# Performance work log

Hardware: AMD Instinct MI355X
Metric: run time of the kernel (lower is better)

## Reference

```python
import jax, jax.numpy as jnp
import numpy as np

EPS = 1e-5

def group_points(feat, idx):
    # feat: [B, C, N1], idx: [B, N2, K] -> [B, C, N2, K]
    return jax.vmap(lambda f, i: f[:, i])(feat, idx)

def conv_bn_relu(x, W, gamma, beta):
    # 1x1 conv2d (no bias) + training-mode BatchNorm2d + ReLU
    y = jnp.einsum('oc,bcnk->bonk', W, x)
    mean = y.mean(axis=(0, 2, 3), keepdims=True)
    var = y.var(axis=(0, 2, 3), keepdims=True)  # biased, as BN uses for normalization
    y = (y - mean) * jax.lax.rsqrt(var + EPS)
    y = y * gamma[None, :, None, None] + beta[None, :, None, None]
    return jax.nn.relu(y)

def setup_inputs() -> dict:
    key = jax.random.key(0)
    ks = jax.random.split(key, 12)
    B, N1, N2, K, C1 = 16, 4096, 1024, 32, 64
    mlp = [C1 + 3, 64, 64, 128]  # use_xyz adds 3 channels
    inp = {
        'in_xyz': jax.random.normal(ks[0], (B, 3, N1), jnp.float32),
        'out_xyz': jax.random.normal(ks[1], (B, 3, N2), jnp.float32),
        'in_feature': jax.random.normal(ks[2], (B, C1, N1), jnp.float32),
        'nbr_index': jax.random.randint(ks[3], (B, N2, K), 0, N1, jnp.int32),
    }
    for li in range(3):
        cin, cout = mlp[li], mlp[li + 1]
        inp[f'W{li}'] = jax.random.normal(ks[4 + li], (cout, cin), jnp.float32) * (1.0 / np.sqrt(cin))
        inp[f'g{li}'] = jnp.ones((cout,), jnp.float32)
        inp[f'b{li}'] = jnp.zeros((cout,), jnp.float32)
    return inp

def reference(in_xyz, out_xyz, in_feature, nbr_index,
              W0, g0, b0, W1, g1, b1, W2, g2, b2):
    # gather neighbor features: [B, C1, N2, K]
    nbr_feature = group_points(in_feature, nbr_index)
    # gather neighbor xyz, recenter on query points: [B, 3, N2, K]
    nbr_xyz = group_points(in_xyz, nbr_index) - out_xyz[:, :, :, None]
    x = jnp.concatenate([nbr_feature, nbr_xyz], axis=1)  # [B, C1+3, N2, K]
    x = conv_bn_relu(x, W0, g0, b0)
    x = conv_bn_relu(x, W1, g1, b1)
    x = conv_bn_relu(x, W2, g2, b2)
    return jnp.max(x, axis=3)  # [B, C2, N2]
```

## Files before the change

### kernel.cpp

```cpp
#include <hip/hip_runtime.h>
#include <cstdint>

typedef unsigned short u16;
typedef unsigned int   u32;
typedef __attribute__((ext_vector_type(8))) short  short8;
typedef __attribute__((ext_vector_type(4))) float  floatx4;

#define NPTS 524288

__device__ __forceinline__ float b2f(u16 h) { return __uint_as_float(((u32)h) << 16); }
__device__ __forceinline__ u16 f2b(float f) {
  u32 u = __float_as_uint(f);
  return (u16)((u + 0x7FFFu + ((u >> 16) & 1u)) >> 16);
}
__device__ __forceinline__ u32 pk_bf16(float lo, float hi) {
  return (u32)f2b(lo) | ((u32)f2b(hi) << 16);
}
__device__ __forceinline__ short8 ld_frag8(const u16* p) {
  union { uint4 q; short8 s; } x;
  x.q = *(const uint4*)p;
  return x.s;
}
__device__ __forceinline__ void bar_lds() {
  asm volatile("s_waitcnt lgkmcnt(0)\n\ts_barrier" ::: "memory");
}

__global__ __launch_bounds__(256) void prep_all(const float* __restrict__ inf,
                                                const float* __restrict__ ixyz,
                                                const float* __restrict__ W0,
                                                const float* __restrict__ W1,
                                                const float* __restrict__ W2,
                                                u16* __restrict__ featT,
                                                float4* __restrict__ xyzT,
                                                u16* __restrict__ Wb) {
  __shared__ float tile[32 * 33];
  const int bk = blockIdx.x, t = threadIdx.x;
  if (bk < 4096) {
    int b = bk >> 8, rem = bk & 255, cc = rem >> 7, nc = rem & 127;
    #pragma unroll
    for (int i = 0; i < 4; ++i) {
      int flat = t + i * 256;
      int cl = flat >> 5, nl = flat & 31;
      tile[cl * 33 + nl] = inf[(size_t)((b * 64) + cc * 32 + cl) * 4096 + nc * 32 + nl];
    }
    __syncthreads();
    #pragma unroll
    for (int i = 0; i < 4; ++i) {
      int flat = t + i * 256;
      int nl = flat >> 5, cl = flat & 31;
      featT[(size_t)((b << 12) + nc * 32 + nl) * 64 + cc * 32 + cl] = f2b(tile[cl * 33 + nl]);
    }
  } else if (bk < 4352) {
    int g = (bk - 4096) * 256 + t;
    int b = g >> 12, n = g & 4095;
    const float* p = ixyz + (size_t)b * 12288;
    xyzT[g] = make_float4(p[n], p[4096 + n], p[8192 + n], 0.f);
  } else {
    int s = (bk - 4352) * 256 + t;
    u16 v = 0;
    if (s < 6656)       { int o = s / 104, c = s % 104; if (c < 67) v = f2b(W0[o * 67 + c]); }
    else if (s < 11264) { int q = s - 6656;  int o = q / 72, c = q % 72; if (c < 64) v = f2b(W1[o * 64 + c]); }
    else                { int q = s - 11264; int o = q / 72, c = q % 72; if (c < 64) v = f2b(W2[o * 64 + c]); }
    Wb[s] = v;
  }
}

template<int KSTEPS, int OCH, bool GATHER, bool MAXOUT>
__global__ __launch_bounds__(256, 4) void gemm_layer(
    const u16* __restrict__ xsrc, const float4* __restrict__ xyzT,
    const float* __restrict__ oxyz, const int* __restrict__ nbr,
    const u16* __restrict__ Wb, const float* __restrict__ ssin,
    u16* __restrict__ yout, u32* __restrict__ gm,
    float* __restrict__ partial) {
  constexpr int PITCH = KSTEPS * 32 + 8;
  __shared__ __align__(16) u16 xs[2][64 * PITCH];
  __shared__ float red[512];
  __shared__ float ss[GATHER ? 4 : 128];

  const int t = threadIdx.x, blk = blockIdx.x;
  const int lane = t & 63, wv = t >> 6, lr = lane & 15, quad = lane >> 4;
  const int m = t >> 2, s4 = t & 3;
  const int P0 = blk * 256;
  const int b = blk >> 7;
  const int rg = wv >> 1, cg = wv & 1;

  short8 wf[4][KSTEPS];
  #pragma unroll
  for (int nt = 0; nt < 4; ++nt) {
    const int orow = (MAXOUT ? cg * 64 : 0) + nt * 16 + lr;
    const u16* wr = Wb + orow * PITCH + quad * 8;
    #pragma unroll
    for (int ks = 0; ks < KSTEPS; ++ks)
      wf[nt][ks] = ld_frag8(wr + ks * 32);
  }

  if constexpr (!GATHER) {
    if (t < 128) ss[t] = ssin[t];
  }
  if constexpr (GATHER) {
    #pragma unroll
    for (int bu = 0; bu < 2; ++bu) {
      if (s4 == 1) {
        u16* xr = xs[bu] + m * PITCH;
        xr[67] = 0;
        #pragma unroll
        for (int j = 0; j < 9; ++j) *(uint2*)(xr + 68 + j * 4) = make_uint2(0u, 0u);
      }
    }
  }
  if constexpr (!GATHER) __syncthreads();

  int idx4[4];
  if constexpr (GATHER) {
    #pragma unroll
    for (int sub = 0; sub < 4; ++sub) idx4[sub] = nbr[P0 + sub * 64 + m];
  }

  uint4 f0, f1;
  float DX = 0.f, DY = 0.f, DZ = 0.f;

  auto issue = [&](int sub) {
    const int P = P0 + sub * 64 + m;
    if constexpr (GATHER) {
      const int id = idx4[sub];
      const u16* row = xsrc + ((size_t)((b << 12) + id)) * 64;
      f0 = *(const uint4*)(row + s4 * 16);
      f1 = *(const uint4*)(row + s4 * 16 + 8);
      if (s4 == 0) {
        const int n2 = (P & 32767) >> 5;
        float4 p = xyzT[(b << 12) + id];
        DX = p.x - oxyz[(b * 3 + 0) * 1024 + n2];
        DY = p.y - oxyz[(b * 3 + 1) * 1024 + n2];
        DZ = p.z - oxyz[(b * 3 + 2) * 1024 + n2];
      }
    } else {
      const u16* row = xsrc + ((size_t)P << 6);
      f0 = *(const uint4*)(row + s4 * 16);
      f1 = *(const uint4*)(row + s4 * 16 + 8);
    }
  };

  auto commit = [&](int bu) {
    u16* xrow = xs[bu] + m * PITCH + s4 * 16;
    if constexpr (GATHER) {
      *(uint4*)(xrow + 0) = f0;
      *(uint4*)(xrow + 8) = f1;
      if (s4 == 0) {
        u16* xr = xs[bu] + m * PITCH;
        xr[64] = f2b(DX); xr[65] = f2b(DY); xr[66] = f2b(DZ);
      }
    } else {
      u32 w[8] = { f0.x, f0.y, f0.z, f0.w, f1.x, f1.y, f1.z, f1.w };
      u32 o[8];
      #pragma unroll
      for (int i = 0; i < 8; ++i) {
        const int c = s4 * 16 + i * 2;
        float lo = fmaxf(b2f((u16)(w[i] & 0xffffu)) * ss[c]     + ss[64 + c],     0.f);
        float hi = fmaxf(b2f((u16)(w[i] >> 16))     * ss[c + 1] + ss[64 + c + 1], 0.f);
        o[i] = pk_bf16(lo, hi);
      }
      *(uint4*)(xrow + 0) = make_uint4(o[0], o[1], o[2], o[3]);
      *(uint4*)(xrow + 8) = make_uint4(o[4], o[5], o[6], o[7]);
    }
  };

  issue(0); commit(0);
  issue(1);
  __syncthreads();

  float s1[4] = {0.f, 0.f, 0.f, 0.f}, s2[4] = {0.f, 0.f, 0.f, 0.f};
  u32* yo = (u32*)yout;

  for (int sub = 0; sub < 4; ++sub) {
    const int cur = sub & 1;
    if (sub < 3) commit(cur ^ 1);
    if (sub < 2) issue(sub + 2);

    if constexpr (!MAXOUT) {
      const u16* ap = xs[cur] + (wv * 16 + lr) * PITCH + quad * 8;
      floatx4 acc[4];
      #pragma unroll
      for (int nt = 0; nt < 4; ++nt) acc[nt] = (floatx4){0.f, 0.f, 0.f, 0.f};
      #pragma unroll
      for (int ks = 0; ks < KSTEPS; ++ks) {
        short8 av = ld_frag8(ap + ks * 32);
        #pragma unroll
        for (int nt = 0; nt < 4; ++nt)
          acc[nt] = __builtin_amdgcn_mfma_f32_16x16x32_bf16(av, wf[nt][ks], acc[nt], 0, 0, 0);
      }
      const int R0 = P0 + sub * 64 + wv * 16 + quad * 4;
      #pragma unroll
      for (int nt = 0; nt < 4; ++nt) {
        #pragma unroll
        for (int r = 0; r < 4; ++r) {
          float v = acc[nt][r];
          s1[nt] += v; s2[nt] += v * v;
          float vo = __shfl_xor(v, 1);
          if ((lr & 1) == 0)
            yo[(size_t)(R0 + r) * 32 + nt * 8 + (lr >> 1)] = pk_bf16(v, vo);
        }
      }
    } else {
      short8 av[2][KSTEPS];
      #pragma unroll
      for (int h = 0; h < 2; ++h)
        #pragma unroll
        for (int ks = 0; ks < KSTEPS; ++ks)
          av[h][ks] = ld_frag8(xs[cur] + (rg * 32 + h * 16 + lr) * PITCH + quad * 8 + ks * 32);
      floatx4 acc[2][4];
      #pragma unroll
      for (int h = 0; h < 2; ++h)
        #pragma unroll
        for (int nt = 0; nt < 4; ++nt) acc[h][nt] = (floatx4){0.f, 0.f, 0.f, 0.f};
      #pragma unroll
      for (int ks = 0; ks < KSTEPS; ++ks)
        #pragma unroll
        for (int nt = 0; nt < 4; ++nt)
          #pragma unroll
          for (int h = 0; h < 2; ++h)
            acc[h][nt] = __builtin_amdgcn_mfma_f32_16x16x32_bf16(av[h][ks], wf[nt][ks], acc[h][nt], 0, 0, 0);
      float mx[4], mn[4];
      #pragma unroll
      for (int nt = 0; nt < 4; ++nt) {
        mx[nt] = -INFINITY; mn[nt] = INFINITY;
        #pragma unroll
        for (int h = 0; h < 2; ++h)
          #pragma unroll
          for (int r = 0; r < 4; ++r) {
            float v = acc[h][nt][r];
            s1[nt] += v; s2[nt] += v * v;
            mx[nt] = fmaxf(mx[nt], v); mn[nt] = fminf(mn[nt], v);
          }
        mx[nt] = fmaxf(mx[nt], __shfl_xor(mx[nt], 16));
        mx[nt] = fmaxf(mx[nt], __shfl_xor(mx[nt], 32));
        mn[nt] = fminf(mn[nt], __shfl_xor(mn[nt], 16));
        mn[nt] = fminf(mn[nt], __shfl_xor(mn[nt], 32));
      }
      if (lane < 16) {
        const int grp = blk * 8 + sub * 2 + rg;
        #pragma unroll
        for (int nt = 0; nt < 4; ++nt)
          gm[(size_t)grp * 128 + cg * 64 + nt * 16 + lr] = pk_bf16(mx[nt], mn[nt]);
      }
    }
    if (sub < 3) bar_lds();
  }

  #pragma unroll
  for (int nt = 0; nt < 4; ++nt) {
    s1[nt] += __shfl_xor(s1[nt], 16); s1[nt] += __shfl_xor(s1[nt], 32);
    s2[nt] += __shfl_xor(s2[nt], 16); s2[nt] += __shfl_xor(s2[nt], 32);
  }
  if (lane < 16) {
    #pragma unroll
    for (int nt = 0; nt < 4; ++nt) {
      red[wv * 64 + nt * 16 + lr] = s1[nt];
      red[256 + wv * 64 + nt * 16 + lr] = s2[nt];
    }
  }
  __syncthreads();
  if constexpr (!MAXOUT) {
    if (t < 64) {
      partial[(size_t)blk * 128 + t] = red[t] + red[64 + t] + red[128 + t] + red[192 + t];
    } else if (t < 128) {
      int c = t - 64;
      partial[(size_t)blk * 128 + t] = red[256 + c] + red[320 + c] + red[384 + c] + red[448 + c];
    }
  } else {
    if (t < 128) {
      int half = t >> 6, i = t & 63;
      partial[(size_t)blk * 256 + t] = red[half * 64 + i] + red[(half + 2) * 64 + i];
    } else {
      int c = t - 128, half = c >> 6, i = c & 63;
      partial[(size_t)blk * 256 + t] = red[256 + half * 64 + i] + red[256 + (half + 2) * 64 + i];
    }
  }
}

__global__ __launch_bounds__(256) void reduce1(const float* __restrict__ partial,
                                               float* __restrict__ tmp, int cols) {
  int c = threadIdx.x;
  if (c >= cols) return;
  int r0 = blockIdx.x * 32;
  float s = 0.f;
  for (int r = 0; r < 32; ++r) s += partial[(size_t)(r0 + r) * cols + c];
  tmp[blockIdx.x * cols + c] = s;
}

__global__ __launch_bounds__(256) void finalize2(const float* __restrict__ tmp,
                                                 const float* __restrict__ gam,
                                                 const float* __restrict__ bet,
                                                 float* __restrict__ ssout, int och) {
  __shared__ float l[256];
  int t = threadIdx.x, cols = 2 * och;
  if (t < cols) {
    float s = 0.f;
    for (int r = 0; r < 64; ++r) s += tmp[r * cols + t];
    l[t] = s;
  }
  __syncthreads();
  if (t < och) {
    const float invN = 1.f / (float)NPTS;
    float mean = l[t] * invN;
    float var  = fmaxf(l[och + t] * invN - mean * mean, 0.f);
    float scale = gam[t] * rsqrtf(var + 1e-5f);
    ssout[t] = scale;
    ssout[och + t] = bet[t] - mean * scale;
  }
}

__global__ __launch_bounds__(256) void final_out(const u32* __restrict__ gm,
                                                 const float* __restrict__ ss2,
                                                 float* __restrict__ out) {
  __shared__ float tile[64 * 33];
  int blk = blockIdx.x;
  int b = blk >> 6, rem = blk & 63, cc = rem >> 4, nn = rem & 15;
  int t = threadIdx.x;
  #pragma unroll
  for (int i = 0; i < 8; ++i) {
    int flat = t + i * 256;
    int n2l = flat >> 5, cl = flat & 31;
    int c = cc * 32 + cl;
    size_t idx = (size_t)((b << 10) + nn * 64 + n2l) * 128 + c;
    u32 p = gm[idx];
    float mx = b2f((u16)(p & 0xffffu)), mn = b2f((u16)(p >> 16));
    float scv = ss2[c], shv = ss2[128 + c];
    float v = (scv >= 0.f) ? mx : mn;
    tile[n2l * 33 + cl] = fmaxf(scv * v + shv, 0.f);
  }
  __syncthreads();
  #pragma unroll
  for (int i = 0; i < 8; ++i) {
    int flat = t + i * 256;
    int cl = flat >> 6, n2l = flat & 63;
    out[(size_t)((b * 128) + cc * 32 + cl) * 1024 + nn * 64 + n2l] = tile[n2l * 33 + cl];
  }
}

extern "C" void kernel_launch(void* const* d_in, const int* in_sizes, int n_in,
                              void* d_out, int out_size, void* d_ws, size_t ws_size,
                              hipStream_t stream) {
  const float* in_xyz  = (const float*)d_in[0];
  const float* out_xyz = (const float*)d_in[1];
  const float* in_feat = (const float*)d_in[2];
  const int*   nbr     = (const int*)d_in[3];
  const float* W0 = (const float*)d_in[4];
  const float* g0 = (const float*)d_in[5];
  const float* b0 = (const float*)d_in[6];
  const float* W1 = (const float*)d_in[7];
  const float* g1 = (const float*)d_in[8];
  const float* b1 = (const float*)d_in[9];
  const float* W2 = (const float*)d_in[10];
  const float* g2 = (const float*)d_in[11];
  const float* b2 = (const float*)d_in[12];
  float* out = (float*)d_out;

  char* ws = (char*)d_ws;
  float*  ssbuf = (float*)(ws + 0);
  u16*    Wb    = (u16*)(ws + 4096);
  float*  tmpA  = (float*)(ws + 65536);
  u16*    featT = (u16*)(ws + 262144);
  float4* xyzT  = (float4*)(ws + 8650752);
  u16*    y0    = (u16*)(ws + 9699328);
  u16*    y1    = (u16*)(ws + 76808192);
  float*  p0    = (float*)(ws + 76808192);
  float*  p1    = (float*)(ws + 262144);
  u32*    gm    = (u32*)(ws + 9699328);
  float*  p2    = (float*)(ws + 9699328 + 8388608);

  hipLaunchKernelGGL(prep_all, dim3(4432), dim3(256), 0, stream,
                     in_feat, in_xyz, W0, W1, W2, featT, xyzT, Wb);

  hipLaunchKernelGGL((gemm_layer<3, 64, true, false>), dim3(2048), dim3(256), 0, stream,
                     featT, xyzT, out_xyz, nbr, Wb, nullptr, y0, nullptr, p0);
  hipLaunchKernelGGL(reduce1, dim3(64), dim3(256), 0, stream, p0, tmpA, 128);
  hipLaunchKernelGGL(finalize2, dim3(1), dim3(256), 0, stream, tmpA, g0, b0, ssbuf, 64);

  hipLaunchKernelGGL((gemm_layer<2, 64, false, false>), dim3(2048), dim3(256), 0, stream,
                     y0, nullptr, nullptr, nullptr, Wb + 6656, ssbuf, y1, nullptr, p1);
  hipLaunchKernelGGL(reduce1, dim3(64), dim3(256), 0, stream, p1, tmpA, 128);
  hipLaunchKernelGGL(finalize2, dim3(1), dim3(256), 0, stream, tmpA, g1, b1, ssbuf + 256, 64);

  hipLaunchKernelGGL((gemm_layer<2, 128, false, true>), dim3(2048), dim3(256), 0, stream,
                     y1, nullptr, nullptr, nullptr, Wb + 11264, ssbuf + 256, nullptr, gm, p2);
  hipLaunchKernelGGL(reduce1, dim3(64), dim3(256), 0, stream, p2, tmpA, 256);
  hipLaunchKernelGGL(finalize2, dim3(1), dim3(256), 0, stream, tmpA, g2, b2, ssbuf + 512, 128);

  hipLaunchKernelGGL(final_out, dim3(1024), dim3(256), 0, stream, gm, ssbuf + 512, out);
}
```

Before: 207.1 us.

## Precompute recentered xyz, deepen gather prefetch, fuse BN reduce and finalize

prep_all now gathers neighbor xyz, subtracts the query point and stores packed bf16 dx/dy/dz per point. The first GEMM then loads one uint2 per row instead of doing a dependent xyzT gather plus three oxyz loads. The gemm loader issues three subtiles ahead through a three-slot register ring so more global loads are in flight. The reduce1 and finalize2 pair is merged into one bn_stats kernel that uses atomicAdd and a last-block counter, removing three launches. In exchange it uses more registers, adds a 4 MB intermediate, and the atomic accumulation order makes the float sums nondeterministic.

```diff
diff --git a/kernel.cpp b/kernel.cpp
--- a/kernel.cpp
+++ b/kernel.cpp
@@ -27,12 +27,16 @@
 
 __global__ __launch_bounds__(256) void prep_all(const float* __restrict__ inf,
                                                 const float* __restrict__ ixyz,
+                                                const float* __restrict__ oxyz,
+                                                const int* __restrict__ nbr,
                                                 const float* __restrict__ W0,
                                                 const float* __restrict__ W1,
                                                 const float* __restrict__ W2,
                                                 u16* __restrict__ featT,
-                                                float4* __restrict__ xyzT,
-                                                u16* __restrict__ Wb) {
+                                                uint2* __restrict__ dxyz,
+                                                u16* __restrict__ Wb,
+                                                u32* __restrict__ cnt,
+                                                float* __restrict__ accz) {
   __shared__ float tile[32 * 33];
   const int bk = blockIdx.x, t = threadIdx.x;
   if (bk < 4096) {
@@ -50,25 +54,35 @@
       int nl = flat >> 5, cl = flat & 31;
       featT[(size_t)((b << 12) + nc * 32 + nl) * 64 + cc * 32 + cl] = f2b(tile[cl * 33 + nl]);
     }
-  } else if (bk < 4352) {
+  } else if (bk < 6144) {
     int g = (bk - 4096) * 256 + t;
-    int b = g >> 12, n = g & 4095;
-    const float* p = ixyz + (size_t)b * 12288;
-    xyzT[g] = make_float4(p[n], p[4096 + n], p[8192 + n], 0.f);
+    int b = g >> 15, r = g & 32767, n2 = r >> 5;
+    int id = nbr[g];
+    const float* ix = ixyz + (size_t)b * 12288;
+    const float* ox = oxyz + (size_t)b * 3072;
+    float dx = ix[id]        - ox[n2];
+    float dy = ix[4096 + id] - ox[1024 + n2];
+    float dzv = ix[8192 + id] - ox[2048 + n2];
+    dxyz[g] = make_uint2(pk_bf16(dx, dy), pk_bf16(dzv, 0.f));
   } else {
-    int s = (bk - 4352) * 256 + t;
+    int s = (bk - 6144) * 256 + t;
     u16 v = 0;
     if (s < 6656)       { int o = s / 104, c = s % 104; if (c < 67) v = f2b(W0[o * 67 + c]); }
     else if (s < 11264) { int q = s - 6656;  int o = q / 72, c = q % 72; if (c < 64) v = f2b(W1[o * 64 + c]); }
     else                { int q = s - 11264; int o = q / 72, c = q % 72; if (c < 64) v = f2b(W2[o * 64 + c]); }
     Wb[s] = v;
+    if (bk == 6144) {
+      if (t < 4) cnt[t] = 0u;
+      accz[t] = 0.f;
+      accz[256 + t] = 0.f;
+    }
   }
 }
 
 template<int KSTEPS, int OCH, bool GATHER, bool MAXOUT>
 __global__ __launch_bounds__(256, 4) void gemm_layer(
-    const u16* __restrict__ xsrc, const float4* __restrict__ xyzT,
-    const float* __restrict__ oxyz, const int* __restrict__ nbr,
+    const u16* __restrict__ xsrc, const uint2* __restrict__ dxyz,
+    const int* __restrict__ nbr,
     const u16* __restrict__ Wb, const float* __restrict__ ssin,
     u16* __restrict__ yout, u32* __restrict__ gm,
     float* __restrict__ partial) {
@@ -102,7 +116,6 @@
     for (int bu = 0; bu < 2; ++bu) {
       if (s4 == 1) {
         u16* xr = xs[bu] + m * PITCH;
-        xr[67] = 0;
         #pragma unroll
         for (int j = 0; j < 9; ++j) *(uint2*)(xr + 68 + j * 4) = make_uint2(0u, 0u);
       }
@@ -116,41 +129,33 @@
     for (int sub = 0; sub < 4; ++sub) idx4[sub] = nbr[P0 + sub * 64 + m];
   }
 
-  uint4 f0, f1;
-  float DX = 0.f, DY = 0.f, DZ = 0.f;
-
-  auto issue = [&](int sub) {
+  uint4 f0[3], f1[3];
+  uint2 dz[3];
+
+  auto issue = [&](int sub, int st) {
     const int P = P0 + sub * 64 + m;
     if constexpr (GATHER) {
       const int id = idx4[sub];
       const u16* row = xsrc + ((size_t)((b << 12) + id)) * 64;
-      f0 = *(const uint4*)(row + s4 * 16);
-      f1 = *(const uint4*)(row + s4 * 16 + 8);
-      if (s4 == 0) {
-        const int n2 = (P & 32767) >> 5;
-        float4 p = xyzT[(b << 12) + id];
-        DX = p.x - oxyz[(b * 3 + 0) * 1024 + n2];
-        DY = p.y - oxyz[(b * 3 + 1) * 1024 + n2];
-        DZ = p.z - oxyz[(b * 3 + 2) * 1024 + n2];
-      }
+      f0[st] = *(const uint4*)(row + s4 * 16);
+      f1[st] = *(const uint4*)(row + s4 * 16 + 8);
+      if (s4 == 0) dz[st] = dxyz[P];
     } else {
       const u16* row = xsrc + ((size_t)P << 6);
-      f0 = *(const uint4*)(row + s4 * 16);
-      f1 = *(const uint4*)(row + s4 * 16 + 8);
+      f0[st] = *(const uint4*)(row + s4 * 16);
+      f1[st] = *(const uint4*)(row + s4 * 16 + 8);
     }
   };
 
-  auto commit = [&](int bu) {
+  auto commit = [&](int bu, int st) {
     u16* xrow = xs[bu] + m * PITCH + s4 * 16;
     if constexpr (GATHER) {
-      *(uint4*)(xrow + 0) = f0;
-      *(uint4*)(xrow + 8) = f1;
-      if (s4 == 0) {
-        u16* xr = xs[bu] + m * PITCH;
-        xr[64] = f2b(DX); xr[65] = f2b(DY); xr[66] = f2b(DZ);
-      }
+      *(uint4*)(xrow + 0) = f0[st];
+      *(uint4*)(xrow + 8) = f1[st];
+      if (s4 == 0) *(uint2*)(xs[bu] + m * PITCH + 64) = dz[st];
     } else {
-      u32 w[8] = { f0.x, f0.y, f0.z, f0.w, f1.x, f1.y, f1.z, f1.w };
+      u32 w[8] = { f0[st].x, f0[st].y, f0[st].z, f0[st].w,
+                   f1[st].x, f1[st].y, f1[st].z, f1[st].w };
       u32 o[8];
       #pragma unroll
       for (int i = 0; i < 8; ++i) {
@@ -164,17 +169,18 @@
     }
   };
 
-  issue(0); commit(0);
-  issue(1);
+  issue(0, 0); issue(1, 1); issue(2, 2);
+  commit(0, 0);
+  issue(3, 0);
   __syncthreads();
 
   float s1[4] = {0.f, 0.f, 0.f, 0.f}, s2[4] = {0.f, 0.f, 0.f, 0.f};
   u32* yo = (u32*)yout;
 
+  #pragma unroll
   for (int sub = 0; sub < 4; ++sub) {
     const int cur = sub & 1;
-    if (sub < 3) commit(cur ^ 1);
-    if (sub < 2) issue(sub + 2);
+    if (sub < 3) commit(cur ^ 1, (sub + 1) % 3);
 
     if constexpr (!MAXOUT) {
       const u16* ap = xs[cur] + (wv * 16 + lr) * PITCH + quad * 8;
@@ -277,27 +283,28 @@
   }
 }
 
-__global__ __launch_bounds__(256) void reduce1(const float* __restrict__ partial,
-                                               float* __restrict__ tmp, int cols) {
-  int c = threadIdx.x;
-  if (c >= cols) return;
-  int r0 = blockIdx.x * 32;
-  float s = 0.f;
-  for (int r = 0; r < 32; ++r) s += partial[(size_t)(r0 + r) * cols + c];
-  tmp[blockIdx.x * cols + c] = s;
-}
-
-__global__ __launch_bounds__(256) void finalize2(const float* __restrict__ tmp,
-                                                 const float* __restrict__ gam,
-                                                 const float* __restrict__ bet,
-                                                 float* __restrict__ ssout, int och) {
+__global__ __launch_bounds__(256) void bn_stats(const float* __restrict__ partial,
+                                                float* __restrict__ accv,
+                                                const float* __restrict__ gam,
+                                                const float* __restrict__ bet,
+                                                float* __restrict__ ssout,
+                                                u32* __restrict__ counter, int och) {
   __shared__ float l[256];
-  int t = threadIdx.x, cols = 2 * och;
+  __shared__ u32 rank;
+  const int cols = 2 * och, t = threadIdx.x;
   if (t < cols) {
+    const size_t r0 = (size_t)blockIdx.x * 32;
     float s = 0.f;
-    for (int r = 0; r < 64; ++r) s += tmp[r * cols + t];
-    l[t] = s;
-  }
+    for (int r = 0; r < 32; ++r) s += partial[(r0 + r) * cols + t];
+    atomicAdd(&accv[t], s);
+  }
+  __threadfence();
+  __syncthreads();
+  if (t == 0) rank = atomicAdd(counter, 1u);
+  __syncthreads();
+  if (rank != 63) return;
+  __threadfence();
+  if (t < cols) l[t] = accv[t];
   __syncthreads();
   if (t < och) {
     const float invN = 1.f / (float)NPTS;
@@ -357,34 +364,35 @@
 
   char* ws = (char*)d_ws;
   float*  ssbuf = (float*)(ws + 0);
-  u16*    Wb    = (u16*)(ws + 4096);
-  float*  tmpA  = (float*)(ws + 65536);
+  u32*    cnt   = (u32*)(ws + 3072);
+  float*  accv  = (float*)(ws + 3584);
+  u16*    Wb    = (u16*)(ws + 8192);
   u16*    featT = (u16*)(ws + 262144);
-  float4* xyzT  = (float4*)(ws + 8650752);
-  u16*    y0    = (u16*)(ws + 9699328);
-  u16*    y1    = (u16*)(ws + 76808192);
-  float*  p0    = (float*)(ws + 76808192);
+  uint2*  dxyz  = (uint2*)(ws + 8650752);
+  u16*    y0    = (u16*)(ws + 13631488);
+  u16*    y1    = (u16*)(ws + 80740352);
+  float*  p0    = (float*)(ws + 80740352);
   float*  p1    = (float*)(ws + 262144);
-  u32*    gm    = (u32*)(ws + 9699328);
-  float*  p2    = (float*)(ws + 9699328 + 8388608);
-
-  hipLaunchKernelGGL(prep_all, dim3(4432), dim3(256), 0, stream,
-                     in_feat, in_xyz, W0, W1, W2, featT, xyzT, Wb);
+  u32*    gm    = (u32*)(ws + 13631488);
+  float*  p2    = (float*)(ws + 13631488 + 8388608);
+
+  hipLaunchKernelGGL(prep_all, dim3(6224), dim3(256), 0, stream,
+                     in_feat, in_xyz, out_xyz, nbr, W0, W1, W2, featT, dxyz, Wb, cnt, accv);
 
   hipLaunchKernelGGL((gemm_layer<3, 64, true, false>), dim3(2048), dim3(256), 0, stream,
-                     featT, xyzT, out_xyz, nbr, Wb, nullptr, y0, nullptr, p0);
-  hipLaunchKernelGGL(reduce1, dim3(64), dim3(256), 0, stream, p0, tmpA, 128);
-  hipLaunchKernelGGL(finalize2, dim3(1), dim3(256), 0, stream, tmpA, g0, b0, ssbuf, 64);
+                     featT, dxyz, nbr, Wb, nullptr, y0, nullptr, p0);
+  hipLaunchKernelGGL(bn_stats, dim3(64), dim3(256), 0, stream,
+                     p0, accv, g0, b0, ssbuf, cnt, 64);
 
   hipLaunchKernelGGL((gemm_layer<2, 64, false, false>), dim3(2048), dim3(256), 0, stream,
-                     y0, nullptr, nullptr, nullptr, Wb + 6656, ssbuf, y1, nullptr, p1);
-  hipLaunchKernelGGL(reduce1, dim3(64), dim3(256), 0, stream, p1, tmpA, 128);
-  hipLaunchKernelGGL(finalize2, dim3(1), dim3(256), 0, stream, tmpA, g1, b1, ssbuf + 256, 64);
+                     y0, nullptr, nullptr, Wb + 6656, ssbuf, y1, nullptr, p1);
+  hipLaunchKernelGGL(bn_stats, dim3(64), dim3(256), 0, stream,
+                     p1, accv + 128, g1, b1, ssbuf + 256, cnt + 1, 64);
 
   hipLaunchKernelGGL((gemm_layer<2, 128, false, true>), dim3(2048), dim3(256), 0, stream,
-                     y1, nullptr, nullptr, nullptr, Wb + 11264, ssbuf + 256, nullptr, gm, p2);
-  hipLaunchKernelGGL(reduce1, dim3(64), dim3(256), 0, stream, p2, tmpA, 256);
-  hipLaunchKernelGGL(finalize2, dim3(1), dim3(256), 0, stream, tmpA, g2, b2, ssbuf + 512, 128);
+                     y1, nullptr, nullptr, Wb + 11264, ssbuf + 256, nullptr, gm, p2);
+  hipLaunchKernelGGL(bn_stats, dim3(64), dim3(256), 0, stream,
+                     p2, accv + 256, g2, b2, ssbuf + 512, cnt + 2, 128);
 
   hipLaunchKernelGGL(final_out, dim3(1024), dim3(256), 0, stream, gm, ssbuf + 512, out);
 }
```

Result: slower. 254.0 us (+22.7%).
